# Kernel optimization log

Hardware: AMD Instinct MI355X
Metric: run time of the kernel (lower is better)

Reference implementation:

```python
import jax, jax.numpy as jnp
import numpy as np

D_MODEL = 1024
NUM_HEADS = 16
D_HEAD = D_MODEL // NUM_HEADS
BATCH, SEQ, MEM = 2, 1024, 1024
TOT = SEQ + MEM


def setup_inputs() -> dict:
    key = jax.random.key(0)
    ks = jax.random.split(key, 16)
    s = 0.02
    return {
        "x": jax.random.normal(ks[0], (BATCH, SEQ, D_MODEL), jnp.float32),
        "mem": jax.random.normal(ks[1], (BATCH, MEM, D_MODEL), jnp.float32),
        "mask": jnp.zeros((1, 1, SEQ, TOT), jnp.float32),
        "rel_enc": jax.random.normal(ks[2], (TOT, D_MODEL), jnp.float32),
        "Wq": jax.random.normal(ks[3], (D_MODEL, D_MODEL), jnp.float32) * s,
        "bq": jnp.zeros((D_MODEL,), jnp.float32),
        "Wke": jax.random.normal(ks[4], (D_MODEL, D_MODEL), jnp.float32) * s,
        "bke": jnp.zeros((D_MODEL,), jnp.float32),
        "Wkr": jax.random.normal(ks[5], (D_MODEL, D_MODEL), jnp.float32) * s,
        "bkr": jnp.zeros((D_MODEL,), jnp.float32),
        "Wv": jax.random.normal(ks[6], (D_MODEL, D_MODEL), jnp.float32) * s,
        "bv": jnp.zeros((D_MODEL,), jnp.float32),
        "Wo": jax.random.normal(ks[7], (D_MODEL, D_MODEL), jnp.float32) * s,
        "bo": jnp.zeros((D_MODEL,), jnp.float32),
    }


def _split_heads(t, b):
    # (b, s, d_model) -> (b, h, s, d_head)
    return t.reshape(b, -1, NUM_HEADS, D_HEAD).transpose(0, 2, 1, 3)


def _rel_enc_shift(arr):
    # arr: (b, h, l, m) -> Transformer-XL shift trick
    b, h, l, m = arr.shape
    arr = jnp.concatenate([arr, jnp.zeros((b, h, l, 1), arr.dtype)], axis=-1)
    arr = arr.reshape(b, h, l * (m + 1))
    return arr[:, :, l - 1:-1].reshape(b, h, l, m)


def reference(x, mem, mask, rel_enc, Wq, bq, Wke, bke, Wkr, bkr, Wv, bv, Wo, bo):
    b, s, _ = x.shape
    x_tilde = jnp.concatenate([mem, x], axis=1)  # (b, tot, d)
    q = _split_heads(x @ Wq + bq, b)             # (b, h, s, dh)
    k = _split_heads(x_tilde @ Wke + bke, b)     # (b, h, tot, dh)
    v = _split_heads(x_tilde @ Wv + bv, b)       # (b, h, tot, dh)
    A = jnp.einsum("bhsd,bhtd->bhst", q, k)      # content scores
    Q = (rel_enc @ Wkr + bkr).reshape(-1, NUM_HEADS, D_HEAD).transpose(1, 0, 2)  # (h, tot, dh)
    B_hat = jnp.einsum("bhsd,htd->bhst", q, Q)
    B = _rel_enc_shift(B_hat)                    # relative-position scores
    scores = (A + B) / jnp.sqrt(jnp.float32(D_HEAD)) + mask * -1e9
    w = jax.nn.softmax(scores, axis=-1)
    out = jnp.einsum("bhst,bhtd->bhsd", w, v)
    out = out.transpose(0, 2, 1, 3).reshape(b, s, D_MODEL)
    return out @ Wo + bo
```

## Files before the change

kernel.cpp:

```cpp
#include <hip/hip_runtime.h>

typedef unsigned short ushort;
typedef unsigned int uint;
typedef __attribute__((ext_vector_type(8))) short short8;
typedef __attribute__((ext_vector_type(4))) float float4v;

#define D_MODEL 1024
#define NH 16
#define DH 64
#define BATCH 2
#define SEQ 1024
#define MEMLEN 1024
#define TOT 2048

__device__ __forceinline__ float b2f(ushort u) {
  return __uint_as_float(((uint)u) << 16);
}
__device__ __forceinline__ ushort f2b(float f) {
  uint i = __float_as_uint(f);
  uint r = (i + 0x7fffu + ((i >> 16) & 1u)) >> 16;
  return (ushort)r;
}
__device__ __forceinline__ void gld16(const ushort* g, ushort* l) {
  __builtin_amdgcn_global_load_lds(
      (const __attribute__((address_space(1))) void*)g,
      (__attribute__((address_space(3))) void*)l, 16, 0, 0);
}

__global__ __launch_bounds__(256) void concat_cvt_kernel(
    const float* __restrict__ x, const float* __restrict__ mem,
    ushort* __restrict__ xt, ushort* __restrict__ xb) {
  int idx = blockIdx.x * 256 + threadIdx.x;
  int row = idx >> 7;
  int c8 = (idx & 127) << 3;
  int b = row >> 11;
  int i = row & 2047;
  const float* src = (i < MEMLEN) ? &mem[((b << 10) + i) * D_MODEL]
                                  : &x[((b << 10) + (i - MEMLEN)) * D_MODEL];
  float4 f0 = *(const float4*)(&src[c8]);
  float4 f1 = *(const float4*)(&src[c8 + 4]);
  ushort u[8] = {f2b(f0.x), f2b(f0.y), f2b(f0.z), f2b(f0.w),
                 f2b(f1.x), f2b(f1.y), f2b(f1.z), f2b(f1.w)};
  *(uint4*)(&xt[row * D_MODEL + c8]) = *(const uint4*)u;
  if (i >= MEMLEN)
    *(uint4*)(&xb[((b << 10) + (i - MEMLEN)) * D_MODEL + c8]) = *(const uint4*)u;
}

__global__ __launch_bounds__(256) void cvt_kernel(const float* __restrict__ in,
                                                  ushort* __restrict__ out) {
  int idx = blockIdx.x * 256 + threadIdx.x;
  int base = idx << 3;
  float4 f0 = *(const float4*)(&in[base]);
  float4 f1 = *(const float4*)(&in[base + 4]);
  ushort u[8] = {f2b(f0.x), f2b(f0.y), f2b(f0.z), f2b(f0.w),
                 f2b(f1.x), f2b(f1.y), f2b(f1.z), f2b(f1.w)};
  *(uint4*)(&out[base]) = *(const uint4*)u;
}

__global__ __launch_bounds__(256) void maskcvt_kernel(
    const float* __restrict__ in, ushort* __restrict__ out) {
  int idx = blockIdx.x * 256 + threadIdx.x;
  int base = idx << 3;
  float4 f0 = *(const float4*)(&in[base]);
  float4 f1 = *(const float4*)(&in[base + 4]);
  ushort u[8] = {f2b(f0.x * -1e9f), f2b(f0.y * -1e9f), f2b(f0.z * -1e9f),
                 f2b(f0.w * -1e9f), f2b(f1.x * -1e9f), f2b(f1.y * -1e9f),
                 f2b(f1.z * -1e9f), f2b(f1.w * -1e9f)};
  *(uint4*)(&out[base]) = *(const uint4*)u;
}

__global__ __launch_bounds__(256) void transpose_cvt5_kernel(
    const float* __restrict__ W0, const float* __restrict__ W1,
    const float* __restrict__ W2, const float* __restrict__ W3,
    const float* __restrict__ W4, ushort* __restrict__ T0,
    ushort* __restrict__ T1, ushort* __restrict__ T2, ushort* __restrict__ T3,
    ushort* __restrict__ T4) {
  __shared__ ushort tle[32][33];
  const float* W;
  ushort* T;
  switch (blockIdx.z) {
    case 0: W = W0; T = T0; break;
    case 1: W = W1; T = T1; break;
    case 2: W = W2; T = T2; break;
    case 3: W = W3; T = T3; break;
    default: W = W4; T = T4; break;
  }
  const int bx = blockIdx.x * 32, by = blockIdx.y * 32;
  const int tx = threadIdx.x & 31, ty = threadIdx.x >> 5;
#pragma unroll
  for (int j = 0; j < 32; j += 8)
    tle[ty + j][tx] = f2b(W[(by + ty + j) * 1024 + bx + tx]);
  __syncthreads();
#pragma unroll
  for (int j = 0; j < 32; j += 8)
    T[(bx + ty + j) * 1024 + by + tx] = tle[tx][ty + j];
}

__global__ __launch_bounds__(256) void vtrans_kernel(
    const ushort* __restrict__ kv, ushort* __restrict__ vt) {
  __shared__ ushort tle[32][76];
  const int gx = blockIdx.x;
  const int gy = blockIdx.y;
  const int tid = threadIdx.x;
  const int r = tid >> 3, c8 = (tid & 7) * 8;
  *(uint4*)(&tle[r][c8]) =
      *(const uint4*)(&kv[(gx * 32 + r) * 2048 + 1024 + gy * 64 + c8]);
  __syncthreads();
  const int dr = tid >> 2, tc8 = (tid & 3) * 8;
  const int bb = (gx * 32) >> 11, tbase = (gx * 32) & 2047;
  ushort tmp[8];
#pragma unroll
  for (int j = 0; j < 8; ++j) tmp[j] = tle[tc8 + j][dr];
  *(uint4*)(&vt[((bb << 10) + gy * 64 + dr) * 2048 + tbase + tc8]) =
      *(const uint4*)tmp;
}

__global__ __launch_bounds__(256) void gemm128_kernel(
    const ushort* __restrict__ A, const ushort* __restrict__ BT,
    const float* __restrict__ b0, const float* __restrict__ b1,
    ushort* __restrict__ Cout, int M, int N, int K) {
  __shared__ ushort As[128 * 32];
  __shared__ ushort Bs[128 * 32];
  const int m0 = blockIdx.x * 128, n0 = blockIdx.y * 128;
  const int tid = threadIdx.x;
  const int w = tid >> 6, lane = tid & 63, m15 = lane & 15, q4 = lane >> 4;
  const int wm = w & 1, wn = w >> 1;
  float4v acc[4][4] = {};
  const int c0 = tid, c1 = tid + 256;
  const int r0 = c0 >> 2, u0 = (c0 & 3) * 8;
  const int r1 = c1 >> 2, u1 = (c1 & 3) * 8;

  for (int kk = 0; kk < K; kk += 32) {
    __syncthreads();
    gld16(&A[(m0 + r0) * K + kk + u0], &As[c0 * 8]);
    gld16(&A[(m0 + r1) * K + kk + u1], &As[c1 * 8]);
    gld16(&BT[(n0 + r0) * K + kk + u0], &Bs[c0 * 8]);
    gld16(&BT[(n0 + r1) * K + kk + u1], &Bs[c1 * 8]);
    __syncthreads();
    short8 af[4], bf[4];
#pragma unroll
    for (int i = 0; i < 4; ++i)
      af[i] = *(const short8*)(&As[(wm * 64 + i * 16 + m15) * 32 + q4 * 8]);
#pragma unroll
    for (int j = 0; j < 4; ++j)
      bf[j] = *(const short8*)(&Bs[(wn * 64 + j * 16 + m15) * 32 + q4 * 8]);
#pragma unroll
    for (int i = 0; i < 4; ++i)
#pragma unroll
      for (int j = 0; j < 4; ++j)
        acc[i][j] =
            __builtin_amdgcn_mfma_f32_16x16x32_bf16(af[i], bf[j], acc[i][j], 0, 0, 0);
  }
#pragma unroll
  for (int j = 0; j < 4; ++j) {
    int col = n0 + wn * 64 + j * 16 + m15;
    float bv = (col < 1024) ? b0[col] : b1[col - 1024];
    float sc = (col < 1024) ? 0.125f : 1.0f;
#pragma unroll
    for (int i = 0; i < 4; ++i) {
      int rowb = m0 + wm * 64 + i * 16 + q4 * 4;
#pragma unroll
      for (int r = 0; r < 4; ++r)
        Cout[(rowb + r) * N + col] = f2b((acc[i][j][r] + bv) * sc);
    }
  }
}

template <int EPI>
__global__ __launch_bounds__(256) void gemm64_kernel(
    const ushort* __restrict__ A, const ushort* __restrict__ BT0,
    const ushort* __restrict__ BT1, int rowSplit, const float* __restrict__ b0,
    const float* __restrict__ b1, void* __restrict__ Cout, int M, int N, int K) {
  __shared__ ushort As[64 * 32];
  __shared__ ushort Bs[128 * 32];
  const int m0 = blockIdx.x * 64, n0 = blockIdx.y * 128;
  const ushort* BT = (m0 < rowSplit) ? BT0 : BT1;
  const float* bias = (m0 < rowSplit) ? b0 : b1;
  const int tid = threadIdx.x;
  const int w = tid >> 6, lane = tid & 63, m15 = lane & 15, q4 = lane >> 4;
  float4v acc[4][2] = {};
  const int ra = tid >> 2, ua = (tid & 3) * 8;
  const int c0 = tid, c1 = tid + 256;
  const int rb0 = c0 >> 2, ub0 = (c0 & 3) * 8;
  const int rb1 = c1 >> 2, ub1 = (c1 & 3) * 8;

  for (int kk = 0; kk < K; kk += 32) {
    __syncthreads();
    gld16(&A[(m0 + ra) * K + kk + ua], &As[tid * 8]);
    gld16(&BT[(n0 + rb0) * K + kk + ub0], &Bs[c0 * 8]);
    gld16(&BT[(n0 + rb1) * K + kk + ub1], &Bs[c1 * 8]);
    __syncthreads();
    short8 bf[2];
#pragma unroll
    for (int j = 0; j < 2; ++j)
      bf[j] = *(const short8*)(&Bs[(w * 32 + j * 16 + m15) * 32 + q4 * 8]);
#pragma unroll
    for (int i = 0; i < 4; ++i) {
      short8 af = *(const short8*)(&As[(i * 16 + m15) * 32 + q4 * 8]);
#pragma unroll
      for (int j = 0; j < 2; ++j)
        acc[i][j] =
            __builtin_amdgcn_mfma_f32_16x16x32_bf16(af, bf[j], acc[i][j], 0, 0, 0);
    }
  }
#pragma unroll
  for (int j = 0; j < 2; ++j) {
    int col = n0 + w * 32 + j * 16 + m15;
    float bv = bias[col];
#pragma unroll
    for (int i = 0; i < 4; ++i) {
      int rowb = m0 + i * 16 + q4 * 4;
#pragma unroll
      for (int r = 0; r < 4; ++r) {
        float v = acc[i][j][r] + bv;
        if (EPI == 1)
          ((float*)Cout)[(rowb + r) * N + col] = v;
        else
          ((ushort*)Cout)[(rowb + r) * N + col] = f2b(v);
      }
    }
  }
}

__global__ __launch_bounds__(256) void bhat_kernel(
    const ushort* __restrict__ q, const ushort* __restrict__ Qrb,
    ushort* __restrict__ Bh) {
  __shared__ ushort As[2 * 128 * 32];
  __shared__ ushort Bs[2 * 128 * 32];
  const int bs0 = blockIdx.x * 128, u0 = blockIdx.y * 128, h = blockIdx.z;
  const int tid = threadIdx.x;
  const int w = tid >> 6, lane = tid & 63, m15 = lane & 15, q4 = lane >> 4;
  const int wm = w & 1, wn = w >> 1;

#pragma unroll
  for (int c = 0; c < 4; ++c) {
    int unit = c * 256 + tid;
    int row = (unit >> 2) & 127, kh = unit >> 9, cu = unit & 3;
    gld16(&q[(bs0 + row) * 1024 + (h << 6) + kh * 32 + cu * 8], &As[unit * 8]);
    gld16(&Qrb[(u0 + row) * 1024 + (h << 6) + kh * 32 + cu * 8], &Bs[unit * 8]);
  }
  __syncthreads();

  float4v acc[4][4] = {};
#pragma unroll
  for (int kh = 0; kh < 2; ++kh) {
    short8 af[4], bf[4];
#pragma unroll
    for (int i = 0; i < 4; ++i)
      af[i] = *(const short8*)(&As[kh * 4096 + (wm * 64 + i * 16 + m15) * 32 + q4 * 8]);
#pragma unroll
    for (int j = 0; j < 4; ++j)
      bf[j] = *(const short8*)(&Bs[kh * 4096 + (wn * 64 + j * 16 + m15) * 32 + q4 * 8]);
#pragma unroll
    for (int i = 0; i < 4; ++i)
#pragma unroll
      for (int j = 0; j < 4; ++j)
        acc[i][j] =
            __builtin_amdgcn_mfma_f32_16x16x32_bf16(af[i], bf[j], acc[i][j], 0, 0, 0);
  }
  const int b = bs0 >> 10;
  const int outrow0 = ((b << 4) + h) * 1024 + (bs0 & 1023);
#pragma unroll
  for (int j = 0; j < 4; ++j) {
    int col = u0 + wn * 64 + j * 16 + m15;
#pragma unroll
    for (int i = 0; i < 4; ++i) {
      int rowb = outrow0 + wm * 64 + i * 16 + q4 * 4;
#pragma unroll
      for (int r = 0; r < 4; ++r)
        Bh[(rowb + r) * 2048 + col] = f2b(acc[i][j][r] * 0.125f);
    }
  }
}

__global__ __launch_bounds__(256) void attn_kernel(
    const ushort* __restrict__ qb, const ushort* __restrict__ kv,
    const ushort* __restrict__ vt, const ushort* __restrict__ Bh,
    const ushort* __restrict__ maskb, ushort* __restrict__ attn) {
  __shared__ ushort Pp[4][16 * 36];
  __shared__ float comb[2][16][68];
  __shared__ float csum[32];

  const int tid = threadIdx.x;
  const int w = tid >> 6, lane = tid & 63, m15 = lane & 15, q4 = lane >> 4;
  const int st = w & 1, th = w >> 1;
  const int s0w = blockIdx.x * 32 + st * 16;
  const int h = blockIdx.y, b = blockIdx.z;
  const int s_l = q4 * 4;

  const ushort* qp = &qb[((b << 10) + s0w + m15) * 1024 + (h << 6) + q4 * 8];
  const short8 af0 = *(const short8*)qp;
  const short8 af1 = *(const short8*)(qp + 32);

  const ushort* kvb = &kv[((size_t)(b << 11) * 2048) + (h << 6)];
  const ushort* vtb = &vt[((size_t)((b << 10) + (h << 6))) * 2048];
  const int bhbase = ((b << 4) + h) << 21;
  ushort* pw = &Pp[w][0];

  ushort bhr[8];
  auto pre_bh = [&](int t0) {
#pragma unroll
    for (int nt = 0; nt < 2; ++nt)
#pragma unroll
      for (int i = 0; i < 4; ++i) {
        int s = s0w + s_l + i;
        int t = t0 + nt * 16 + m15;
        int u = t - s + 1023;
        int row = (u <= 2047) ? s : (s + 1);
        int uu = (u <= 2047) ? u : (u - 2049);
        ushort v = Bh[bhbase + (row << 11) + uu];
        bhr[nt * 4 + i] = (u == 2048) ? (ushort)0 : v;
      }
  };

  float lsum4[4] = {0.f, 0.f, 0.f, 0.f};
  float4v oacc[4] = {};
  pre_bh(th * 1024);

  for (int ci = 0; ci < 32; ++ci) {
    const int t0 = th * 1024 + ci * 32;
    short8 Kr[2][2], Vr[4];
    ushort mk[8];
#pragma unroll
    for (int nt = 0; nt < 2; ++nt) {
      const ushort* kp = &kvb[(size_t)(t0 + nt * 16 + m15) * 2048 + q4 * 8];
      Kr[nt][0] = *(const short8*)kp;
      Kr[nt][1] = *(const short8*)(kp + 32);
    }
#pragma unroll
    for (int nd = 0; nd < 4; ++nd)
      Vr[nd] = *(const short8*)(&vtb[(size_t)(nd * 16 + m15) * 2048 + t0 + q4 * 8]);
#pragma unroll
    for (int nt = 0; nt < 2; ++nt)
#pragma unroll
      for (int i = 0; i < 4; ++i)
        mk[nt * 4 + i] = maskb[(s0w + s_l + i) * 2048 + t0 + nt * 16 + m15];
    ushort bhc[8];
#pragma unroll
    for (int j = 0; j < 8; ++j) bhc[j] = bhr[j];
    if (ci < 31) pre_bh(t0 + 32);

#pragma unroll
    for (int nt = 0; nt < 2; ++nt) {
      float4v a = {0.f, 0.f, 0.f, 0.f};
      a = __builtin_amdgcn_mfma_f32_16x16x32_bf16(af0, Kr[nt][0], a, 0, 0, 0);
      a = __builtin_amdgcn_mfma_f32_16x16x32_bf16(af1, Kr[nt][1], a, 0, 0, 0);
#pragma unroll
      for (int i = 0; i < 4; ++i) {
        float p = __expf(a[i] + b2f(bhc[nt * 4 + i]) + b2f(mk[nt * 4 + i]));
        lsum4[i] += p;
        pw[(s_l + i) * 36 + nt * 16 + m15] = f2b(p);
      }
    }
    short8 pfr = *(const short8*)(&pw[m15 * 36 + q4 * 8]);
#pragma unroll
    for (int nd = 0; nd < 4; ++nd)
      oacc[nd] = __builtin_amdgcn_mfma_f32_16x16x32_bf16(pfr, Vr[nd], oacc[nd], 0, 0, 0);
  }

#pragma unroll
  for (int i = 0; i < 4; ++i) {
    float v = lsum4[i];
    v += __shfl_xor(v, 1, 64);
    v += __shfl_xor(v, 2, 64);
    v += __shfl_xor(v, 4, 64);
    v += __shfl_xor(v, 8, 64);
    lsum4[i] = v;
  }
  if (th == 1) {
#pragma unroll
    for (int nd = 0; nd < 4; ++nd)
#pragma unroll
      for (int i = 0; i < 4; ++i)
        comb[st][s_l + i][nd * 16 + m15] = oacc[nd][i];
    if (m15 == 0)
#pragma unroll
      for (int i = 0; i < 4; ++i) csum[st * 16 + s_l + i] = lsum4[i];
  }
  __syncthreads();
  if (th == 0) {
#pragma unroll
    for (int i = 0; i < 4; ++i) lsum4[i] += csum[st * 16 + s_l + i];
#pragma unroll
    for (int nd = 0; nd < 4; ++nd)
#pragma unroll
      for (int i = 0; i < 4; ++i) {
        float v = oacc[nd][i] + comb[st][s_l + i][nd * 16 + m15];
        attn[((b << 10) + s0w + s_l + i) * 1024 + (h << 6) + nd * 16 + m15] =
            f2b(v / lsum4[i]);
      }
  }
}

extern "C" void kernel_launch(void* const* d_in, const int* in_sizes, int n_in,
                              void* d_out, int out_size, void* d_ws,
                              size_t ws_size, hipStream_t stream) {
  const float* x = (const float*)d_in[0];
  const float* mem = (const float*)d_in[1];
  const float* mask = (const float*)d_in[2];
  const float* rel = (const float*)d_in[3];
  const float* Wq = (const float*)d_in[4];
  const float* bq = (const float*)d_in[5];
  const float* Wke = (const float*)d_in[6];
  const float* bke = (const float*)d_in[7];
  const float* Wkr = (const float*)d_in[8];
  const float* bkr = (const float*)d_in[9];
  const float* Wv = (const float*)d_in[10];
  const float* bv = (const float*)d_in[11];
  const float* Wo = (const float*)d_in[12];
  const float* bo = (const float*)d_in[13];
  float* out = (float*)d_out;

  ushort* ws = (ushort*)d_ws;
  ushort* xt = ws;
  ushort* xbrel = xt + 4096 * 1024;
  ushort* WqT = xbrel + 4096 * 1024;
  ushort* WkeT = WqT + 1024 * 1024;
  ushort* WvT = WkeT + 1024 * 1024;
  ushort* WkrT = WvT + 1024 * 1024;
  ushort* WoT = WkrT + 1024 * 1024;
  ushort* kv = WoT + 1024 * 1024;
  ushort* qr = kv + 4096 * 2048;
  ushort* attn = qr + 4096 * 1024;
  ushort* maskb = attn + 2048 * 1024;
  ushort* Bh = maskb + 1024 * 2048;
  ushort* relb = xbrel + 2048 * 1024;
  ushort* Qrb = qr + 2048 * 1024;
  ushort* vt = xt;

  concat_cvt_kernel<<<2048, 256, 0, stream>>>(x, mem, xt, xbrel);
  cvt_kernel<<<1024, 256, 0, stream>>>(rel, relb);
  maskcvt_kernel<<<1024, 256, 0, stream>>>(mask, maskb);
  transpose_cvt5_kernel<<<dim3(32, 32, 5), 256, 0, stream>>>(
      Wq, Wke, Wkr, Wv, Wo, WqT, WkeT, WkrT, WvT, WoT);

  gemm128_kernel<<<dim3(32, 16), 256, 0, stream>>>(xt, WkeT, bke, bv, kv,
                                                   4096, 2048, 1024);
  gemm64_kernel<0><<<dim3(64, 8), 256, 0, stream>>>(
      xbrel, WqT, WkrT, 2048, bq, bkr, qr, 4096, 1024, 1024);
  vtrans_kernel<<<dim3(128, 16), 256, 0, stream>>>(kv, vt);

  bhat_kernel<<<dim3(16, 16, 16), 256, 0, stream>>>(qr, Qrb, Bh);

  attn_kernel<<<dim3(SEQ / 32, NH, BATCH), 256, 0, stream>>>(
      qr, kv, vt, Bh, maskb, attn);

  gemm64_kernel<1><<<dim3(32, 8), 256, 0, stream>>>(
      attn, WoT, WoT, 1 << 30, bo, bo, out, 2048, 1024, 1024);
}
```

Before: 364.7 us.

## Apply rel-shift and mask in bhat epilogue; double-buffer attention loads

The B_hat kernel now writes its scores directly at their shifted Transformer-XL positions and adds the mask there, so the attention kernel reads one pre-shifted, pre-masked bias tile with simple contiguous indexing. This replaces the per-element shift index arithmetic and the separate mask load in the inner loop. A small extra kernel fills the diagonal entries that the shift leaves zero with the mask value. The attention loop also becomes explicitly double-buffered over K/V/bias chunks, which adds register pressure. Epilogue stores in bhat become scattered, and each one needs an extra mask read.

```diff
diff --git a/kernel.cpp b/kernel.cpp
--- a/kernel.cpp
+++ b/kernel.cpp
@@ -224,7 +224,7 @@
 
 __global__ __launch_bounds__(256) void bhat_kernel(
     const ushort* __restrict__ q, const ushort* __restrict__ Qrb,
-    ushort* __restrict__ Bh) {
+    const ushort* __restrict__ maskb, ushort* __restrict__ Bsh) {
   __shared__ ushort As[2 * 128 * 32];
   __shared__ ushort Bs[2 * 128 * 32];
   const int bs0 = blockIdx.x * 128, u0 = blockIdx.y * 128, h = blockIdx.z;
@@ -259,24 +259,43 @@
             __builtin_amdgcn_mfma_f32_16x16x32_bf16(af[i], bf[j], acc[i][j], 0, 0, 0);
   }
   const int b = bs0 >> 10;
-  const int outrow0 = ((b << 4) + h) * 1024 + (bs0 & 1023);
+  const int s0loc = bs0 & 1023;
+  const size_t plane = (size_t)((b << 4) + h) * (size_t)(1024 * 2048);
 #pragma unroll
   for (int j = 0; j < 4; ++j) {
-    int col = u0 + wn * 64 + j * 16 + m15;
+    int u = u0 + wn * 64 + j * 16 + m15;
 #pragma unroll
     for (int i = 0; i < 4; ++i) {
-      int rowb = outrow0 + wm * 64 + i * 16 + q4 * 4;
-#pragma unroll
-      for (int r = 0; r < 4; ++r)
-        Bh[(rowb + r) * 2048 + col] = f2b(acc[i][j][r] * 0.125f);
-    }
-  }
+      int sp0 = s0loc + wm * 64 + i * 16 + q4 * 4;
+#pragma unroll
+      for (int r = 0; r < 4; ++r) {
+        int sp = sp0 + r;
+        int sel = (u + sp >= 1023) ? 1 : 0;
+        int row = sp - 1 + sel;
+        int t = u + sp - 1023 + (sel ? 0 : 2048);
+        if (row >= 0) {
+          float mval = b2f(maskb[row * 2048 + t]);
+          Bsh[plane + (size_t)row * 2048 + t] =
+              f2b(acc[i][j][r] * 0.125f + mval);
+        }
+      }
+    }
+  }
+}
+
+__global__ __launch_bounds__(256) void zdiag_kernel(
+    const ushort* __restrict__ maskb, ushort* __restrict__ Bsh) {
+  int idx = blockIdx.x * 256 + threadIdx.x;
+  int plane = idx >> 10, s = idx & 1023;
+  if (s >= 1023) return;
+  int t = s + 1025;
+  Bsh[(size_t)plane * (size_t)(1024 * 2048) + s * 2048 + t] = maskb[s * 2048 + t];
 }
 
 __global__ __launch_bounds__(256) void attn_kernel(
     const ushort* __restrict__ qb, const ushort* __restrict__ kv,
-    const ushort* __restrict__ vt, const ushort* __restrict__ Bh,
-    const ushort* __restrict__ maskb, ushort* __restrict__ attn) {
+    const ushort* __restrict__ vt, const ushort* __restrict__ Bsh,
+    ushort* __restrict__ attn) {
   __shared__ ushort Pp[4][16 * 36];
   __shared__ float comb[2][16][68];
   __shared__ float csum[32];
@@ -294,60 +313,43 @@
 
   const ushort* kvb = &kv[((size_t)(b << 11) * 2048) + (h << 6)];
   const ushort* vtb = &vt[((size_t)((b << 10) + (h << 6))) * 2048];
-  const int bhbase = ((b << 4) + h) << 21;
+  const ushort* bshb = &Bsh[(size_t)((b << 4) + h) * (size_t)(1024 * 2048) +
+                            (size_t)(s0w + s_l) * 2048];
   ushort* pw = &Pp[w][0];
-
-  ushort bhr[8];
-  auto pre_bh = [&](int t0) {
-#pragma unroll
-    for (int nt = 0; nt < 2; ++nt)
-#pragma unroll
-      for (int i = 0; i < 4; ++i) {
-        int s = s0w + s_l + i;
-        int t = t0 + nt * 16 + m15;
-        int u = t - s + 1023;
-        int row = (u <= 2047) ? s : (s + 1);
-        int uu = (u <= 2047) ? u : (u - 2049);
-        ushort v = Bh[bhbase + (row << 11) + uu];
-        bhr[nt * 4 + i] = (u == 2048) ? (ushort)0 : v;
-      }
-  };
 
   float lsum4[4] = {0.f, 0.f, 0.f, 0.f};
   float4v oacc[4] = {};
-  pre_bh(th * 1024);
-
-  for (int ci = 0; ci < 32; ++ci) {
-    const int t0 = th * 1024 + ci * 32;
-    short8 Kr[2][2], Vr[4];
-    ushort mk[8];
+
+  short8 K0[2][2], V0[4];
+  short8 K1[2][2], V1[4];
+  ushort B0[8], B1[8];
+
+  auto loadc = [&](int t0, short8 (&K)[2][2], short8 (&V)[4], ushort (&B)[8]) {
 #pragma unroll
     for (int nt = 0; nt < 2; ++nt) {
       const ushort* kp = &kvb[(size_t)(t0 + nt * 16 + m15) * 2048 + q4 * 8];
-      Kr[nt][0] = *(const short8*)kp;
-      Kr[nt][1] = *(const short8*)(kp + 32);
+      K[nt][0] = *(const short8*)kp;
+      K[nt][1] = *(const short8*)(kp + 32);
     }
 #pragma unroll
     for (int nd = 0; nd < 4; ++nd)
-      Vr[nd] = *(const short8*)(&vtb[(size_t)(nd * 16 + m15) * 2048 + t0 + q4 * 8]);
+      V[nd] = *(const short8*)(&vtb[(size_t)(nd * 16 + m15) * 2048 + t0 + q4 * 8]);
 #pragma unroll
     for (int nt = 0; nt < 2; ++nt)
 #pragma unroll
       for (int i = 0; i < 4; ++i)
-        mk[nt * 4 + i] = maskb[(s0w + s_l + i) * 2048 + t0 + nt * 16 + m15];
-    ushort bhc[8];
-#pragma unroll
-    for (int j = 0; j < 8; ++j) bhc[j] = bhr[j];
-    if (ci < 31) pre_bh(t0 + 32);
-
+        B[nt * 4 + i] = bshb[i * 2048 + t0 + nt * 16 + m15];
+  };
+
+  auto computec = [&](short8 (&K)[2][2], short8 (&V)[4], ushort (&B)[8]) {
 #pragma unroll
     for (int nt = 0; nt < 2; ++nt) {
       float4v a = {0.f, 0.f, 0.f, 0.f};
-      a = __builtin_amdgcn_mfma_f32_16x16x32_bf16(af0, Kr[nt][0], a, 0, 0, 0);
-      a = __builtin_amdgcn_mfma_f32_16x16x32_bf16(af1, Kr[nt][1], a, 0, 0, 0);
+      a = __builtin_amdgcn_mfma_f32_16x16x32_bf16(af0, K[nt][0], a, 0, 0, 0);
+      a = __builtin_amdgcn_mfma_f32_16x16x32_bf16(af1, K[nt][1], a, 0, 0, 0);
 #pragma unroll
       for (int i = 0; i < 4; ++i) {
-        float p = __expf(a[i] + b2f(bhc[nt * 4 + i]) + b2f(mk[nt * 4 + i]));
+        float p = __expf(a[i] + b2f(B[nt * 4 + i]));
         lsum4[i] += p;
         pw[(s_l + i) * 36 + nt * 16 + m15] = f2b(p);
       }
@@ -355,7 +357,17 @@
     short8 pfr = *(const short8*)(&pw[m15 * 36 + q4 * 8]);
 #pragma unroll
     for (int nd = 0; nd < 4; ++nd)
-      oacc[nd] = __builtin_amdgcn_mfma_f32_16x16x32_bf16(pfr, Vr[nd], oacc[nd], 0, 0, 0);
+      oacc[nd] = __builtin_amdgcn_mfma_f32_16x16x32_bf16(pfr, V[nd], oacc[nd], 0, 0, 0);
+  };
+
+  const int tb = th * 1024;
+  loadc(tb, K0, V0, B0);
+  for (int ci2 = 0; ci2 < 16; ++ci2) {
+    const int t0 = tb + ci2 * 64;
+    loadc(t0 + 32, K1, V1, B1);
+    computec(K0, V0, B0);
+    if (ci2 < 15) loadc(t0 + 64, K0, V0, B0);
+    computec(K1, V1, B1);
   }
 
 #pragma unroll
@@ -423,7 +435,7 @@
   ushort* qr = kv + 4096 * 2048;
   ushort* attn = qr + 4096 * 1024;
   ushort* maskb = attn + 2048 * 1024;
-  ushort* Bh = maskb + 1024 * 2048;
+  ushort* Bsh = maskb + 1024 * 2048;
   ushort* relb = xbrel + 2048 * 1024;
   ushort* Qrb = qr + 2048 * 1024;
   ushort* vt = xt;
@@ -440,10 +452,11 @@
       xbrel, WqT, WkrT, 2048, bq, bkr, qr, 4096, 1024, 1024);
   vtrans_kernel<<<dim3(128, 16), 256, 0, stream>>>(kv, vt);
 
-  bhat_kernel<<<dim3(16, 16, 16), 256, 0, stream>>>(qr, Qrb, Bh);
+  bhat_kernel<<<dim3(16, 16, 16), 256, 0, stream>>>(qr, Qrb, maskb, Bsh);
+  zdiag_kernel<<<128, 256, 0, stream>>>(maskb, Bsh);
 
   attn_kernel<<<dim3(SEQ / 32, NH, BATCH), 256, 0, stream>>>(
-      qr, kv, vt, Bh, maskb, attn);
+      qr, kv, vt, Bsh, attn);
 
   gemm64_kernel<1><<<dim3(32, 8), 256, 0, stream>>>(
       attn, WoT, WoT, 1 << 30, bo, bo, out, 2048, 1024, 1024);
```

Measured after the change: 406.8 us. +11.6%, slower.

## Fuse relative-position score computation into attention kernel, drop Bh materialization

Applied to the files above, without the earlier changes.

Removes the separate bhat kernel that wrote a full (b,h,s,tot) bf16 relative-score tensor to memory. The attention kernel now recomputes the shifted relative scores on the fly with extra MFMAs against a sliding window of the scaled rel-key projection, staging them in LDS. It also double-buffers the K, rel-key and mask register loads across chunks. This trades a large intermediate write and gather read for extra matrix math and LDS traffic per tile, plus higher register pressure.

```diff
diff --git a/kernel.cpp b/kernel.cpp
--- a/kernel.cpp
+++ b/kernel.cpp
@@ -170,12 +170,14 @@
 __global__ __launch_bounds__(256) void gemm64_kernel(
     const ushort* __restrict__ A, const ushort* __restrict__ BT0,
     const ushort* __restrict__ BT1, int rowSplit, const float* __restrict__ b0,
-    const float* __restrict__ b1, void* __restrict__ Cout, int M, int N, int K) {
+    const float* __restrict__ b1, float sc1, void* __restrict__ Cout, int M,
+    int N, int K) {
   __shared__ ushort As[64 * 32];
   __shared__ ushort Bs[128 * 32];
   const int m0 = blockIdx.x * 64, n0 = blockIdx.y * 128;
   const ushort* BT = (m0 < rowSplit) ? BT0 : BT1;
   const float* bias = (m0 < rowSplit) ? b0 : b1;
+  const float sc = (m0 < rowSplit) ? 1.0f : sc1;
   const int tid = threadIdx.x;
   const int w = tid >> 6, lane = tid & 63, m15 = lane & 15, q4 = lane >> 4;
   float4v acc[4][2] = {};
@@ -212,7 +214,7 @@
       int rowb = m0 + i * 16 + q4 * 4;
 #pragma unroll
       for (int r = 0; r < 4; ++r) {
-        float v = acc[i][j][r] + bv;
+        float v = (acc[i][j][r] + bv) * sc;
         if (EPI == 1)
           ((float*)Cout)[(rowb + r) * N + col] = v;
         else
@@ -222,61 +224,11 @@
   }
 }
 
-__global__ __launch_bounds__(256) void bhat_kernel(
-    const ushort* __restrict__ q, const ushort* __restrict__ Qrb,
-    ushort* __restrict__ Bh) {
-  __shared__ ushort As[2 * 128 * 32];
-  __shared__ ushort Bs[2 * 128 * 32];
-  const int bs0 = blockIdx.x * 128, u0 = blockIdx.y * 128, h = blockIdx.z;
-  const int tid = threadIdx.x;
-  const int w = tid >> 6, lane = tid & 63, m15 = lane & 15, q4 = lane >> 4;
-  const int wm = w & 1, wn = w >> 1;
-
-#pragma unroll
-  for (int c = 0; c < 4; ++c) {
-    int unit = c * 256 + tid;
-    int row = (unit >> 2) & 127, kh = unit >> 9, cu = unit & 3;
-    gld16(&q[(bs0 + row) * 1024 + (h << 6) + kh * 32 + cu * 8], &As[unit * 8]);
-    gld16(&Qrb[(u0 + row) * 1024 + (h << 6) + kh * 32 + cu * 8], &Bs[unit * 8]);
-  }
-  __syncthreads();
-
-  float4v acc[4][4] = {};
-#pragma unroll
-  for (int kh = 0; kh < 2; ++kh) {
-    short8 af[4], bf[4];
-#pragma unroll
-    for (int i = 0; i < 4; ++i)
-      af[i] = *(const short8*)(&As[kh * 4096 + (wm * 64 + i * 16 + m15) * 32 + q4 * 8]);
-#pragma unroll
-    for (int j = 0; j < 4; ++j)
-      bf[j] = *(const short8*)(&Bs[kh * 4096 + (wn * 64 + j * 16 + m15) * 32 + q4 * 8]);
-#pragma unroll
-    for (int i = 0; i < 4; ++i)
-#pragma unroll
-      for (int j = 0; j < 4; ++j)
-        acc[i][j] =
-            __builtin_amdgcn_mfma_f32_16x16x32_bf16(af[i], bf[j], acc[i][j], 0, 0, 0);
-  }
-  const int b = bs0 >> 10;
-  const int outrow0 = ((b << 4) + h) * 1024 + (bs0 & 1023);
-#pragma unroll
-  for (int j = 0; j < 4; ++j) {
-    int col = u0 + wn * 64 + j * 16 + m15;
-#pragma unroll
-    for (int i = 0; i < 4; ++i) {
-      int rowb = outrow0 + wm * 64 + i * 16 + q4 * 4;
-#pragma unroll
-      for (int r = 0; r < 4; ++r)
-        Bh[(rowb + r) * 2048 + col] = f2b(acc[i][j][r] * 0.125f);
-    }
-  }
-}
-
 __global__ __launch_bounds__(256) void attn_kernel(
     const ushort* __restrict__ qb, const ushort* __restrict__ kv,
-    const ushort* __restrict__ vt, const ushort* __restrict__ Bh,
+    const ushort* __restrict__ vt, const ushort* __restrict__ Qrb,
     const ushort* __restrict__ maskb, ushort* __restrict__ attn) {
+  __shared__ float Bt[4][2][16 * 50];
   __shared__ ushort Pp[4][16 * 36];
   __shared__ float comb[2][16][68];
   __shared__ float csum[32];
@@ -291,63 +243,128 @@
   const ushort* qp = &qb[((b << 10) + s0w + m15) * 1024 + (h << 6) + q4 * 8];
   const short8 af0 = *(const short8*)qp;
   const short8 af1 = *(const short8*)(qp + 32);
+  const int srow1 = (s0w + m15 + 1 > 1023) ? 1023 : (s0w + m15 + 1);
+  const ushort* qps = &qb[((b << 10) + srow1) * 1024 + (h << 6) + q4 * 8];
+  const short8 afs0 = *(const short8*)qps;
+  const short8 afs1 = *(const short8*)(qps + 32);
 
   const ushort* kvb = &kv[((size_t)(b << 11) * 2048) + (h << 6)];
   const ushort* vtb = &vt[((size_t)((b << 10) + (h << 6))) * 2048];
-  const int bhbase = ((b << 4) + h) << 21;
   ushort* pw = &Pp[w][0];
-
-  ushort bhr[8];
-  auto pre_bh = [&](int t0) {
+  float* btA = &Bt[w][0][0];
+  float* btB = &Bt[w][1][0];
+
+  float lsum4[4] = {0.f, 0.f, 0.f, 0.f};
+  float4v oacc[4] = {};
+
+  short8 K0[2][2], K1[2][2];
+  short8 QW0[3][2], QW1[3][2];
+  ushort mk0[8], mk1[8];
+
+  auto loadK = [&](int t0, short8 (&K)[2][2]) {
+#pragma unroll
+    for (int nt = 0; nt < 2; ++nt) {
+      const ushort* kp = &kvb[(size_t)(t0 + nt * 16 + m15) * 2048 + q4 * 8];
+      K[nt][0] = *(const short8*)kp;
+      K[nt][1] = *(const short8*)(kp + 32);
+    }
+  };
+  auto loadQW = [&](int t0, short8 (&QW)[3][2]) {
+    const bool pA = (t0 <= s0w + 1039);
+    const int wb = t0 - s0w + (pA ? 1008 : -1041);
+#pragma unroll
+    for (int tt = 0; tt < 3; ++tt) {
+      int wr = wb + tt * 16 + m15;
+      wr = wr < 0 ? 0 : (wr > 2047 ? 2047 : wr);
+      const ushort* qrp = &Qrb[(size_t)wr * 1024 + (h << 6) + q4 * 8];
+      QW[tt][0] = *(const short8*)qrp;
+      QW[tt][1] = *(const short8*)(qrp + 32);
+    }
+  };
+  auto loadMk = [&](int t0, ushort (&mk)[8]) {
 #pragma unroll
     for (int nt = 0; nt < 2; ++nt)
+#pragma unroll
+      for (int i = 0; i < 4; ++i)
+        mk[nt * 4 + i] = maskb[(s0w + s_l + i) * 2048 + t0 + nt * 16 + m15];
+  };
+
+  auto process = [&](int t0, short8 (&K)[2][2], short8 (&QW)[3][2],
+                     ushort (&mk)[8], int pt0, short8 (&Kp)[2][2],
+                     short8 (&QWp)[3][2], ushort (&mkp)[8], bool doPre) {
+    short8 Vr[4];
+#pragma unroll
+    for (int nd = 0; nd < 4; ++nd)
+      Vr[nd] = *(const short8*)(&vtb[(size_t)(nd * 16 + m15) * 2048 + t0 + q4 * 8]);
+    float4v a0 = {}, a1 = {};
+    a0 = __builtin_amdgcn_mfma_f32_16x16x32_bf16(af0, K[0][0], a0, 0, 0, 0);
+    a0 = __builtin_amdgcn_mfma_f32_16x16x32_bf16(af1, K[0][1], a0, 0, 0, 0);
+    a1 = __builtin_amdgcn_mfma_f32_16x16x32_bf16(af0, K[1][0], a1, 0, 0, 0);
+    a1 = __builtin_amdgcn_mfma_f32_16x16x32_bf16(af1, K[1][1], a1, 0, 0, 0);
+    if (doPre) {
+      loadK(pt0, Kp);
+      loadQW(pt0, QWp);
+      loadMk(pt0, mkp);
+    }
+    const bool pA = (t0 <= s0w + 1039);
+    const bool nB = (t0 >= s0w + 995);
+    const short8 pa0 = pA ? af0 : afs0;
+    const short8 pa1 = pA ? af1 : afs1;
+    float4v bh0 = {}, bh1 = {}, bh2 = {};
+    bh0 = __builtin_amdgcn_mfma_f32_16x16x32_bf16(pa0, QW[0][0], bh0, 0, 0, 0);
+    bh0 = __builtin_amdgcn_mfma_f32_16x16x32_bf16(pa1, QW[0][1], bh0, 0, 0, 0);
+    bh1 = __builtin_amdgcn_mfma_f32_16x16x32_bf16(pa0, QW[1][0], bh1, 0, 0, 0);
+    bh1 = __builtin_amdgcn_mfma_f32_16x16x32_bf16(pa1, QW[1][1], bh1, 0, 0, 0);
+    bh2 = __builtin_amdgcn_mfma_f32_16x16x32_bf16(pa0, QW[2][0], bh2, 0, 0, 0);
+    bh2 = __builtin_amdgcn_mfma_f32_16x16x32_bf16(pa1, QW[2][1], bh2, 0, 0, 0);
+    float* btP = pA ? btA : btB;
+#pragma unroll
+    for (int i = 0; i < 4; ++i) {
+      btP[(s_l + i) * 50 + m15] = bh0[i];
+      btP[(s_l + i) * 50 + 16 + m15] = bh1[i];
+      btP[(s_l + i) * 50 + 32 + m15] = bh2[i];
+    }
+    if (pA && nB) {
+      const int vb = t0 - s0w - 1041;
+      float4v bs0 = {}, bs1 = {}, bs2 = {};
+#pragma unroll
+      for (int tt = 0; tt < 3; ++tt) {
+        int wr = vb + tt * 16 + m15;
+        wr = wr < 0 ? 0 : wr;
+        const ushort* qrp = &Qrb[(size_t)wr * 1024 + (h << 6) + q4 * 8];
+        short8 qs0 = *(const short8*)qrp;
+        short8 qs1 = *(const short8*)(qrp + 32);
+        if (tt == 0) {
+          bs0 = __builtin_amdgcn_mfma_f32_16x16x32_bf16(afs0, qs0, bs0, 0, 0, 0);
+          bs0 = __builtin_amdgcn_mfma_f32_16x16x32_bf16(afs1, qs1, bs0, 0, 0, 0);
+        } else if (tt == 1) {
+          bs1 = __builtin_amdgcn_mfma_f32_16x16x32_bf16(afs0, qs0, bs1, 0, 0, 0);
+          bs1 = __builtin_amdgcn_mfma_f32_16x16x32_bf16(afs1, qs1, bs1, 0, 0, 0);
+        } else {
+          bs2 = __builtin_amdgcn_mfma_f32_16x16x32_bf16(afs0, qs0, bs2, 0, 0, 0);
+          bs2 = __builtin_amdgcn_mfma_f32_16x16x32_bf16(afs1, qs1, bs2, 0, 0, 0);
+        }
+      }
+#pragma unroll
+      for (int i = 0; i < 4; ++i) {
+        btB[(s_l + i) * 50 + m15] = bs0[i];
+        btB[(s_l + i) * 50 + 16 + m15] = bs1[i];
+        btB[(s_l + i) * 50 + 32 + m15] = bs2[i];
+      }
+    }
+#pragma unroll
+    for (int nt = 0; nt < 2; ++nt) {
 #pragma unroll
       for (int i = 0; i < 4; ++i) {
         int s = s0w + s_l + i;
         int t = t0 + nt * 16 + m15;
         int u = t - s + 1023;
-        int row = (u <= 2047) ? s : (s + 1);
-        int uu = (u <= 2047) ? u : (u - 2049);
-        ushort v = Bh[bhbase + (row << 11) + uu];
-        bhr[nt * 4 + i] = (u == 2048) ? (ushort)0 : v;
-      }
-  };
-
-  float lsum4[4] = {0.f, 0.f, 0.f, 0.f};
-  float4v oacc[4] = {};
-  pre_bh(th * 1024);
-
-  for (int ci = 0; ci < 32; ++ci) {
-    const int t0 = th * 1024 + ci * 32;
-    short8 Kr[2][2], Vr[4];
-    ushort mk[8];
-#pragma unroll
-    for (int nt = 0; nt < 2; ++nt) {
-      const ushort* kp = &kvb[(size_t)(t0 + nt * 16 + m15) * 2048 + q4 * 8];
-      Kr[nt][0] = *(const short8*)kp;
-      Kr[nt][1] = *(const short8*)(kp + 32);
-    }
-#pragma unroll
-    for (int nd = 0; nd < 4; ++nd)
-      Vr[nd] = *(const short8*)(&vtb[(size_t)(nd * 16 + m15) * 2048 + t0 + q4 * 8]);
-#pragma unroll
-    for (int nt = 0; nt < 2; ++nt)
-#pragma unroll
-      for (int i = 0; i < 4; ++i)
-        mk[nt * 4 + i] = maskb[(s0w + s_l + i) * 2048 + t0 + nt * 16 + m15];
-    ushort bhc[8];
-#pragma unroll
-    for (int j = 0; j < 8; ++j) bhc[j] = bhr[j];
-    if (ci < 31) pre_bh(t0 + 32);
-
-#pragma unroll
-    for (int nt = 0; nt < 2; ++nt) {
-      float4v a = {0.f, 0.f, 0.f, 0.f};
-      a = __builtin_amdgcn_mfma_f32_16x16x32_bf16(af0, Kr[nt][0], a, 0, 0, 0);
-      a = __builtin_amdgcn_mfma_f32_16x16x32_bf16(af1, Kr[nt][1], a, 0, 0, 0);
-#pragma unroll
-      for (int i = 0; i < 4; ++i) {
-        float p = __expf(a[i] + b2f(bhc[nt * 4 + i]) + b2f(mk[nt * 4 + i]));
+        int off = (s_l + i) * 50 + (nt * 16 + m15) - (s_l + i) + 15;
+        const float* bp = (u <= 2047) ? btA : btB;
+        float bval = bp[off];
+        bval = (u == 2048) ? 0.f : bval;
+        float a = (nt == 0) ? a0[i] : a1[i];
+        float p = __expf(a + bval + b2f(mk[nt * 4 + i]));
         lsum4[i] += p;
         pw[(s_l + i) * 36 + nt * 16 + m15] = f2b(p);
       }
@@ -355,7 +372,18 @@
     short8 pfr = *(const short8*)(&pw[m15 * 36 + q4 * 8]);
 #pragma unroll
     for (int nd = 0; nd < 4; ++nd)
-      oacc[nd] = __builtin_amdgcn_mfma_f32_16x16x32_bf16(pfr, Vr[nd], oacc[nd], 0, 0, 0);
+      oacc[nd] =
+          __builtin_amdgcn_mfma_f32_16x16x32_bf16(pfr, Vr[nd], oacc[nd], 0, 0, 0);
+  };
+
+  const int tb = th * 1024;
+  loadK(tb, K0);
+  loadQW(tb, QW0);
+  loadMk(tb, mk0);
+  for (int ci2 = 0; ci2 < 16; ++ci2) {
+    const int t0 = tb + ci2 * 64;
+    process(t0, K0, QW0, mk0, t0 + 32, K1, QW1, mk1, true);
+    process(t0 + 32, K1, QW1, mk1, t0 + 64, K0, QW0, mk0, ci2 < 15);
   }
 
 #pragma unroll
@@ -423,7 +451,6 @@
   ushort* qr = kv + 4096 * 2048;
   ushort* attn = qr + 4096 * 1024;
   ushort* maskb = attn + 2048 * 1024;
-  ushort* Bh = maskb + 1024 * 2048;
   ushort* relb = xbrel + 2048 * 1024;
   ushort* Qrb = qr + 2048 * 1024;
   ushort* vt = xt;
@@ -437,14 +464,12 @@
   gemm128_kernel<<<dim3(32, 16), 256, 0, stream>>>(xt, WkeT, bke, bv, kv,
                                                    4096, 2048, 1024);
   gemm64_kernel<0><<<dim3(64, 8), 256, 0, stream>>>(
-      xbrel, WqT, WkrT, 2048, bq, bkr, qr, 4096, 1024, 1024);
+      xbrel, WqT, WkrT, 2048, bq, bkr, 0.125f, qr, 4096, 1024, 1024);
   vtrans_kernel<<<dim3(128, 16), 256, 0, stream>>>(kv, vt);
 
-  bhat_kernel<<<dim3(16, 16, 16), 256, 0, stream>>>(qr, Qrb, Bh);
-
   attn_kernel<<<dim3(SEQ / 32, NH, BATCH), 256, 0, stream>>>(
-      qr, kv, vt, Bh, maskb, attn);
+      qr, kv, vt, Qrb, maskb, attn);
 
   gemm64_kernel<1><<<dim3(32, 8), 256, 0, stream>>>(
-      attn, WoT, WoT, 1 << 30, bo, bo, out, 2048, 1024, 1024);
-}
+      attn, WoT, WoT, 1 << 30, bo, bo, 1.0f, out, 2048, 1024, 1024);
+}
```

After: 400.5 us. 9.8% more time.

## Fold mask into shifted B_hat in bhat kernel and deepen attention prefetch

Applied to the files above, without the earlier changes.

The bhat kernel now adds the shift-mapped mask value into B_hat as it writes it, so the attention kernel no longer loads the mask per score. The shift index math is simplified to precomputed per-row offsets, with one diagonal element handled specially. The 0.125 scale moves into the Qr projection epilogue. Bh prefetch is deepened from one 32-wide chunk to four via a loop unrolled into phases, which raises register pressure and adds index logic in exchange for fewer global loads and more latency hiding.

```diff
diff --git a/kernel.cpp b/kernel.cpp
--- a/kernel.cpp
+++ b/kernel.cpp
@@ -170,12 +170,14 @@
 __global__ __launch_bounds__(256) void gemm64_kernel(
     const ushort* __restrict__ A, const ushort* __restrict__ BT0,
     const ushort* __restrict__ BT1, int rowSplit, const float* __restrict__ b0,
-    const float* __restrict__ b1, void* __restrict__ Cout, int M, int N, int K) {
+    const float* __restrict__ b1, float sc1, void* __restrict__ Cout, int M,
+    int N, int K) {
   __shared__ ushort As[64 * 32];
   __shared__ ushort Bs[128 * 32];
   const int m0 = blockIdx.x * 64, n0 = blockIdx.y * 128;
   const ushort* BT = (m0 < rowSplit) ? BT0 : BT1;
   const float* bias = (m0 < rowSplit) ? b0 : b1;
+  const float sc = (m0 < rowSplit) ? 1.0f : sc1;
   const int tid = threadIdx.x;
   const int w = tid >> 6, lane = tid & 63, m15 = lane & 15, q4 = lane >> 4;
   float4v acc[4][2] = {};
@@ -212,7 +214,7 @@
       int rowb = m0 + i * 16 + q4 * 4;
 #pragma unroll
       for (int r = 0; r < 4; ++r) {
-        float v = acc[i][j][r] + bv;
+        float v = (acc[i][j][r] + bv) * sc;
         if (EPI == 1)
           ((float*)Cout)[(rowb + r) * N + col] = v;
         else
@@ -224,7 +226,7 @@
 
 __global__ __launch_bounds__(256) void bhat_kernel(
     const ushort* __restrict__ q, const ushort* __restrict__ Qrb,
-    ushort* __restrict__ Bh) {
+    const ushort* __restrict__ maskb, ushort* __restrict__ Bh) {
   __shared__ ushort As[2 * 128 * 32];
   __shared__ ushort Bs[2 * 128 * 32];
   const int bs0 = blockIdx.x * 128, u0 = blockIdx.y * 128, h = blockIdx.z;
@@ -259,16 +261,24 @@
             __builtin_amdgcn_mfma_f32_16x16x32_bf16(af[i], bf[j], acc[i][j], 0, 0, 0);
   }
   const int b = bs0 >> 10;
-  const int outrow0 = ((b << 4) + h) * 1024 + (bs0 & 1023);
+  const int s0loc = bs0 & 1023;
+  const int outrow0 = ((b << 4) + h) * 1024 + s0loc;
 #pragma unroll
   for (int j = 0; j < 4; ++j) {
-    int col = u0 + wn * 64 + j * 16 + m15;
+    int u = u0 + wn * 64 + j * 16 + m15;
 #pragma unroll
     for (int i = 0; i < 4; ++i) {
       int rowb = outrow0 + wm * 64 + i * 16 + q4 * 4;
-#pragma unroll
-      for (int r = 0; r < 4; ++r)
-        Bh[(rowb + r) * 2048 + col] = f2b(acc[i][j][r] * 0.125f);
+      int spb = s0loc + wm * 64 + i * 16 + q4 * 4;
+#pragma unroll
+      for (int r = 0; r < 4; ++r) {
+        int sp = spb + r;
+        bool selA = (u >= 1023 - sp);
+        int mrow = selA ? sp : (sp > 0 ? sp - 1 : 0);
+        int mcol = selA ? (u + sp - 1023) : (u + sp + 1025);
+        float mval = b2f(maskb[mrow * 2048 + mcol]);
+        Bh[(rowb + r) * 2048 + u] = f2b(acc[i][j][r] + mval);
+      }
     }
   }
 }
@@ -297,65 +307,82 @@
   const int bhbase = ((b << 4) + h) << 21;
   ushort* pw = &Pp[w][0];
 
-  ushort bhr[8];
-  auto pre_bh = [&](int t0) {
+  int offA[4], offB[4], diagT[4];
+  float dm[4];
+#pragma unroll
+  for (int i = 0; i < 4; ++i) {
+    int s = s0w + s_l + i;
+    offA[i] = bhbase + (s << 11) - s + 1023;
+    offB[i] = bhbase + ((s + 1) << 11) - s - 1026;
+    diagT[i] = s + 1025;
+    dm[i] = (diagT[i] <= 2047) ? b2f(maskb[s * 2048 + diagT[i]]) : 0.f;
+  }
+
+  float lsum4[4] = {0.f, 0.f, 0.f, 0.f};
+  float4v oacc[4] = {};
+  ushort Bb0[8], Bb1[8], Bb2[8], Bb3[8];
+
+  auto pre_bh = [&](int t0, ushort (&B)[8]) {
 #pragma unroll
     for (int nt = 0; nt < 2; ++nt)
 #pragma unroll
       for (int i = 0; i < 4; ++i) {
-        int s = s0w + s_l + i;
         int t = t0 + nt * 16 + m15;
-        int u = t - s + 1023;
-        int row = (u <= 2047) ? s : (s + 1);
-        int uu = (u <= 2047) ? u : (u - 2049);
-        ushort v = Bh[bhbase + (row << 11) + uu];
-        bhr[nt * 4 + i] = (u == 2048) ? (ushort)0 : v;
+        int off = (t < diagT[i]) ? offA[i] : offB[i];
+        B[nt * 4 + i] = Bh[off + t];
       }
   };
 
-  float lsum4[4] = {0.f, 0.f, 0.f, 0.f};
-  float4v oacc[4] = {};
-  pre_bh(th * 1024);
-
-  for (int ci = 0; ci < 32; ++ci) {
-    const int t0 = th * 1024 + ci * 32;
-    short8 Kr[2][2], Vr[4];
-    ushort mk[8];
+  auto phase = [&](int t0, ushort (&Bb)[8], bool pf) {
+    short8 Vr[4], Kr[2][2];
+#pragma unroll
+    for (int nd = 0; nd < 4; ++nd)
+      Vr[nd] = *(const short8*)(&vtb[(size_t)(nd * 16 + m15) * 2048 + t0 + q4 * 8]);
 #pragma unroll
     for (int nt = 0; nt < 2; ++nt) {
       const ushort* kp = &kvb[(size_t)(t0 + nt * 16 + m15) * 2048 + q4 * 8];
       Kr[nt][0] = *(const short8*)kp;
       Kr[nt][1] = *(const short8*)(kp + 32);
     }
-#pragma unroll
-    for (int nd = 0; nd < 4; ++nd)
-      Vr[nd] = *(const short8*)(&vtb[(size_t)(nd * 16 + m15) * 2048 + t0 + q4 * 8]);
+    ushort cur[8];
+#pragma unroll
+    for (int j = 0; j < 8; ++j) cur[j] = Bb[j];
+    if (pf) pre_bh(t0 + 128, Bb);
+    float4v a0 = {}, a1 = {};
+    a0 = __builtin_amdgcn_mfma_f32_16x16x32_bf16(af0, Kr[0][0], a0, 0, 0, 0);
+    a0 = __builtin_amdgcn_mfma_f32_16x16x32_bf16(af1, Kr[0][1], a0, 0, 0, 0);
+    a1 = __builtin_amdgcn_mfma_f32_16x16x32_bf16(af0, Kr[1][0], a1, 0, 0, 0);
+    a1 = __builtin_amdgcn_mfma_f32_16x16x32_bf16(af1, Kr[1][1], a1, 0, 0, 0);
 #pragma unroll
     for (int nt = 0; nt < 2; ++nt)
 #pragma unroll
-      for (int i = 0; i < 4; ++i)
-        mk[nt * 4 + i] = maskb[(s0w + s_l + i) * 2048 + t0 + nt * 16 + m15];
-    ushort bhc[8];
-#pragma unroll
-    for (int j = 0; j < 8; ++j) bhc[j] = bhr[j];
-    if (ci < 31) pre_bh(t0 + 32);
-
-#pragma unroll
-    for (int nt = 0; nt < 2; ++nt) {
-      float4v a = {0.f, 0.f, 0.f, 0.f};
-      a = __builtin_amdgcn_mfma_f32_16x16x32_bf16(af0, Kr[nt][0], a, 0, 0, 0);
-      a = __builtin_amdgcn_mfma_f32_16x16x32_bf16(af1, Kr[nt][1], a, 0, 0, 0);
-#pragma unroll
       for (int i = 0; i < 4; ++i) {
-        float p = __expf(a[i] + b2f(bhc[nt * 4 + i]) + b2f(mk[nt * 4 + i]));
+        int t = t0 + nt * 16 + m15;
+        float bv = (t == diagT[i]) ? dm[i] : b2f(cur[nt * 4 + i]);
+        float a = (nt == 0) ? a0[i] : a1[i];
+        float p = __expf(a + bv);
         lsum4[i] += p;
         pw[(s_l + i) * 36 + nt * 16 + m15] = f2b(p);
       }
-    }
     short8 pfr = *(const short8*)(&pw[m15 * 36 + q4 * 8]);
 #pragma unroll
     for (int nd = 0; nd < 4; ++nd)
-      oacc[nd] = __builtin_amdgcn_mfma_f32_16x16x32_bf16(pfr, Vr[nd], oacc[nd], 0, 0, 0);
+      oacc[nd] =
+          __builtin_amdgcn_mfma_f32_16x16x32_bf16(pfr, Vr[nd], oacc[nd], 0, 0, 0);
+  };
+
+  const int tb = th * 1024;
+  pre_bh(tb, Bb0);
+  pre_bh(tb + 32, Bb1);
+  pre_bh(tb + 64, Bb2);
+  pre_bh(tb + 96, Bb3);
+  for (int it = 0; it < 8; ++it) {
+    const int t0 = tb + it * 128;
+    const bool pf = (it < 7);
+    phase(t0, Bb0, pf);
+    phase(t0 + 32, Bb1, pf);
+    phase(t0 + 64, Bb2, pf);
+    phase(t0 + 96, Bb3, pf);
   }
 
 #pragma unroll
@@ -437,14 +464,14 @@
   gemm128_kernel<<<dim3(32, 16), 256, 0, stream>>>(xt, WkeT, bke, bv, kv,
                                                    4096, 2048, 1024);
   gemm64_kernel<0><<<dim3(64, 8), 256, 0, stream>>>(
-      xbrel, WqT, WkrT, 2048, bq, bkr, qr, 4096, 1024, 1024);
+      xbrel, WqT, WkrT, 2048, bq, bkr, 0.125f, qr, 4096, 1024, 1024);
   vtrans_kernel<<<dim3(128, 16), 256, 0, stream>>>(kv, vt);
 
-  bhat_kernel<<<dim3(16, 16, 16), 256, 0, stream>>>(qr, Qrb, Bh);
+  bhat_kernel<<<dim3(16, 16, 16), 256, 0, stream>>>(qr, Qrb, maskb, Bh);
 
   attn_kernel<<<dim3(SEQ / 32, NH, BATCH), 256, 0, stream>>>(
       qr, kv, vt, Bh, maskb, attn);
 
   gemm64_kernel<1><<<dim3(32, 8), 256, 0, stream>>>(
-      attn, WoT, WoT, 1 << 30, bo, bo, out, 2048, 1024, 1024);
-}
+      attn, WoT, WoT, 1 << 30, bo, bo, 1.0f, out, 2048, 1024, 1024);
+}
```

New measurement: 371.6 us. Within noise of the previous version (+1.9%).
